# Kernel tuning notes

Hardware: AMD Instinct MI355X
Metric: run time of the kernel (lower is better)

## Reference

```python
import jax, jax.numpy as jnp
import numpy as np

B, S, INPUT_DIM = 8, 2048, 512
D_MODEL, N_LAYERS, OUTPUT_DIM = 1024, 6, 512
LAMBDA_INIT = 0.5


def _sinusoidal_pe(seq_len, d_model):
    # standard sinusoidal positional encoding, added over the sequence dim
    pos = np.arange(seq_len, dtype=np.float32)[:, None]
    div = np.exp(-np.log(10000.0) * np.arange(0, d_model, 2, dtype=np.float32) / d_model)
    pe = np.zeros((seq_len, d_model), dtype=np.float32)
    pe[:, 0::2] = np.sin(pos * div)
    pe[:, 1::2] = np.cos(pos * div)
    return jnp.asarray(pe)


def setup_inputs() -> dict:
    key = jax.random.key(0)
    ks = jax.random.split(key, 10)
    scale = 0.02
    x = jax.random.normal(ks[0], (B, S, INPUT_DIM), dtype=jnp.float32)
    W_in = jax.random.normal(ks[1], (D_MODEL, INPUT_DIM), dtype=jnp.float32) * scale
    b_in = jnp.zeros((D_MODEL,), dtype=jnp.float32)
    W_ctx = jax.random.normal(ks[2], (D_MODEL, D_MODEL), dtype=jnp.float32) * scale
    b_ctx = jnp.zeros((D_MODEL,), dtype=jnp.float32)
    # per-layer in_proj splits: W_q, W_k, W_v each [d_model, d_model]
    Wq = jax.random.normal(ks[3], (N_LAYERS, D_MODEL, D_MODEL), dtype=jnp.float32) * scale
    Wk = jax.random.normal(ks[4], (N_LAYERS, D_MODEL, D_MODEL), dtype=jnp.float32) * scale
    Wv = jax.random.normal(ks[5], (N_LAYERS, D_MODEL, D_MODEL), dtype=jnp.float32) * scale
    W_out = jax.random.normal(ks[6], (OUTPUT_DIM, D_MODEL), dtype=jnp.float32) * scale
    b_out = jnp.zeros((OUTPUT_DIM,), dtype=jnp.float32)
    return {"x": x, "W_in": W_in, "b_in": b_in, "W_ctx": W_ctx, "b_ctx": b_ctx,
            "Wq": Wq, "Wk": Wk, "Wv": Wv, "W_out": W_out, "b_out": b_out}


def _diff_attention(h, W_q, W_k, W_v):
    # h: [B, S, d]; weights used un-transposed, matching X @ W_q in the source
    d = h.shape[-1]
    half = d // 2
    Q = h @ W_q
    K = h @ W_k
    V = h @ W_v
    Q1, Q2 = Q[..., :half], Q[..., half:]
    K1, K2 = K[..., :half], K[..., half:]
    s = 1.0 / jnp.sqrt(jnp.float32(d))
    A1 = jnp.einsum('bqd,bkd->bqk', Q1, K1) * s  # [B, S, S]
    A2 = jnp.einsum('bqd,bkd->bqk', Q2, K2) * s
    scores = jax.nn.softmax(A1, axis=-1) - LAMBDA_INIT * jax.nn.softmax(A2, axis=-1)
    return jnp.einsum('bqk,bkd->bqd', scores, V)


def reference(x, W_in, b_in, W_ctx, b_ctx, Wq, Wk, Wv, W_out, b_out):
    h = x @ W_in.T + b_in            # input_fc
    h = h @ W_ctx.T + b_ctx          # context_embedding
    h = h + _sinusoidal_pe(S, D_MODEL)[None, :, :]
    for i in range(N_LAYERS):
        h = _diff_attention(h, Wq[i], Wk[i], Wv[i])
    return h @ W_out.T + b_out
```

## Files before the change

kernel.cpp:

```cpp
#include <hip/hip_runtime.h>
#include <stdint.h>

typedef unsigned short u16b;
typedef __attribute__((ext_vector_type(8))) __bf16 bf16x8;
typedef __attribute__((ext_vector_type(8))) unsigned short ushort8;
typedef __attribute__((ext_vector_type(4))) float f32x4;

#define B_    8
#define S_    2048
#define DIN_  512
#define DM_   1024
#define NL_   6
#define DOUT_ 512
#define MTOT  (B_ * S_)

__device__ __forceinline__ u16b f2bf(float f) {
  unsigned u = __builtin_bit_cast(unsigned, f);
  u += 0x7fffu + ((u >> 16) & 1u);
  return (u16b)(u >> 16);
}
__device__ __forceinline__ float bf2f(u16b h) {
  return __builtin_bit_cast(float, (unsigned)h << 16);
}

__global__ void pe_kernel(float* __restrict__ pe) {
  int idx = blockIdx.x * 256 + threadIdx.x;
  int s = idx >> 10, d = idx & 1023;
  int j = d >> 1;
  double div = exp(-log(10000.0) * (double)(2 * j) / 1024.0);
  double ang = (double)s * div;
  pe[idx] = (float)((d & 1) ? cos(ang) : sin(ang));
}

__global__ void cvt_bf16(const float* __restrict__ in, u16b* __restrict__ out, long long n) {
  long long i = (long long)blockIdx.x * 256 + threadIdx.x;
  long long st = (long long)gridDim.x * 256;
  for (; i < n; i += st) out[i] = f2bf(in[i]);
}

__global__ void tr3_f32_bf16(const float* __restrict__ q, const float* __restrict__ k,
                             const float* __restrict__ v,
                             u16b* __restrict__ oq, u16b* __restrict__ ok2,
                             u16b* __restrict__ ov) {
  __shared__ float tile[32][33];
  const float* in = blockIdx.z == 0 ? q : (blockIdx.z == 1 ? k : v);
  u16b* out = blockIdx.z == 0 ? oq : (blockIdx.z == 1 ? ok2 : ov);
  int c0 = blockIdx.x * 32, r0 = blockIdx.y * 32;
  int tx = threadIdx.x, ty = threadIdx.y;
#pragma unroll
  for (int i = 0; i < 4; ++i)
    tile[ty + i * 8][tx] = in[(size_t)(r0 + ty + i * 8) * DM_ + c0 + tx];
  __syncthreads();
#pragma unroll
  for (int i = 0; i < 4; ++i)
    out[(size_t)(c0 + ty + i * 8) * DM_ + r0 + tx] = f2bf(tile[tx][ty + i * 8]);
}

__global__ __launch_bounds__(256) void softmax_combine(const float* __restrict__ A1,
                                                       const float* __restrict__ A2,
                                                       u16b* __restrict__ P,
                                                       long long pstride) {
  size_t row = blockIdx.x;
  const float* a1 = A1 + row * 2048;
  const float* a2 = A2 + row * 2048;
  u16b* p = P + row * pstride;
  int t = threadIdx.x, w = t >> 6, lane = t & 63;
  float v1[8], v2[8];
  float m1 = -3.4e38f, m2 = -3.4e38f;
#pragma unroll
  for (int i = 0; i < 8; ++i) {
    v1[i] = a1[i * 256 + t];
    v2[i] = a2[i * 256 + t];
    m1 = fmaxf(m1, v1[i]);
    m2 = fmaxf(m2, v2[i]);
  }
  __shared__ float red1[4], red2[4];
#pragma unroll
  for (int o = 32; o; o >>= 1) {
    m1 = fmaxf(m1, __shfl_xor(m1, o));
    m2 = fmaxf(m2, __shfl_xor(m2, o));
  }
  if (lane == 0) { red1[w] = m1; red2[w] = m2; }
  __syncthreads();
  m1 = fmaxf(fmaxf(red1[0], red1[1]), fmaxf(red1[2], red1[3]));
  m2 = fmaxf(fmaxf(red2[0], red2[1]), fmaxf(red2[2], red2[3]));
  float s1 = 0.f, s2 = 0.f;
#pragma unroll
  for (int i = 0; i < 8; ++i) {
    v1[i] = expf(v1[i] - m1);
    v2[i] = expf(v2[i] - m2);
    s1 += v1[i];
    s2 += v2[i];
  }
#pragma unroll
  for (int o = 32; o; o >>= 1) {
    s1 += __shfl_xor(s1, o);
    s2 += __shfl_xor(s2, o);
  }
  __syncthreads();
  if (lane == 0) { red1[w] = s1; red2[w] = s2; }
  __syncthreads();
  s1 = red1[0] + red1[1] + red1[2] + red1[3];
  s2 = red2[0] + red2[1] + red2[2] + red2[3];
  float i1 = 1.0f / s1, i2 = 0.5f / s2;
#pragma unroll
  for (int i = 0; i < 8; ++i)
    p[i * 256 + t] = f2bf(v1[i] * i1 - v2[i] * i2);
}

__global__ __launch_bounds__(256) void softmax_quad(const u16b* __restrict__ A1b,
                                                    const u16b* __restrict__ A2b,
                                                    u16b* __restrict__ P, int quadBase) {
  int row = blockIdx.x;
  int bb = row >> 11, r = row & 2047;
  size_t ro = (size_t)bb * S_ * S_ + (size_t)r * S_;
  const u16b* a1 = A1b + ro;
  const u16b* a2 = A2b + ro;
  u16b* p = P + (size_t)(quadBase + bb) * S_ * S_ + (size_t)r * S_;
  int t = threadIdx.x, w = t >> 6, lane = t & 63;
  ushort8 x1 = *(const ushort8*)&a1[t * 8];
  ushort8 x2 = *(const ushort8*)&a2[t * 8];
  float v1[8], v2[8];
  float m1 = -3.4e38f, m2 = -3.4e38f;
#pragma unroll
  for (int i = 0; i < 8; ++i) {
    v1[i] = bf2f(x1[i]);
    v2[i] = bf2f(x2[i]);
    m1 = fmaxf(m1, v1[i]);
    m2 = fmaxf(m2, v2[i]);
  }
  __shared__ float red1[4], red2[4];
#pragma unroll
  for (int o = 32; o; o >>= 1) {
    m1 = fmaxf(m1, __shfl_xor(m1, o));
    m2 = fmaxf(m2, __shfl_xor(m2, o));
  }
  if (lane == 0) { red1[w] = m1; red2[w] = m2; }
  __syncthreads();
  m1 = fmaxf(fmaxf(red1[0], red1[1]), fmaxf(red1[2], red1[3]));
  m2 = fmaxf(fmaxf(red2[0], red2[1]), fmaxf(red2[2], red2[3]));
  float s1 = 0.f, s2 = 0.f;
#pragma unroll
  for (int i = 0; i < 8; ++i) {
    v1[i] = expf(v1[i] - m1);
    v2[i] = expf(v2[i] - m2);
    s1 += v1[i];
    s2 += v2[i];
  }
#pragma unroll
  for (int o = 32; o; o >>= 1) {
    s1 += __shfl_xor(s1, o);
    s2 += __shfl_xor(s2, o);
  }
  __syncthreads();
  if (lane == 0) { red1[w] = s1; red2[w] = s2; }
  __syncthreads();
  s1 = red1[0] + red1[1] + red1[2] + red1[3];
  s2 = red2[0] + red2[1] + red2[2] + red2[3];
  float i1 = 1.0f / s1, i2 = 0.5f / s2;
  ushort8 outv;
#pragma unroll
  for (int i = 0; i < 8; ++i) outv[i] = f2bf(v1[i] * i1 - v2[i] * i2);
  *(ushort8*)&p[t * 8] = outv;
}

#define GEPI_BF16      0
#define GEPI_BIAS      1
#define GEPI_BIAS_PE   2
#define GEPI_F32SCALE  3
#define GEPI_F32BIAS   4
#define GEPI_BF16_VT   5
#define GEPI_BF16SCALE 6

template <int EPI>
__global__ __launch_bounds__(256) void gemm_nt(
    const u16b* __restrict__ A, long long sAr, long long sAb,
    const u16b* __restrict__ Bt, long long sBr, long long sBb,
    void* __restrict__ Cv, long long sCr, long long sCb,
    int K, const float* __restrict__ bias, const float* __restrict__ pe, float alpha) {
  __shared__ __align__(16) u16b smem[16384];
  u16b* As = smem;
  u16b* Bs = smem + 8192;
  const int z = blockIdx.z;
  const u16b* Ab = A + (size_t)z * sAb;
  const u16b* Bb = Bt + (size_t)z * sBb;
  const int m0 = blockIdx.x * 128, n0 = blockIdx.y * 128;
  const int t = threadIdx.x;
  const int w = t >> 6, lane = t & 63;
  const int wr = w >> 1, wc = w & 1;
  const int lr = lane & 15, g0 = lane >> 4;

  f32x4 acc[4][4] = {};

  const int nkt = K >> 6;
  for (int kt = 0; kt < nkt; ++kt) {
#pragma unroll
    for (int i = 0; i < 4; ++i) {
      int c = i * 256 + t;
      int r = c >> 3, cc = c & 7;
      int gc = cc ^ (r & 7);
      const u16b* ga = Ab + (size_t)(m0 + r) * sAr + kt * 64 + gc * 8;
      const u16b* gb = Bb + (size_t)(n0 + r) * sBr + kt * 64 + gc * 8;
      u16b* la = &As[(i * 256 + w * 64) * 8];
      u16b* lb = &Bs[(i * 256 + w * 64) * 8];
      __builtin_amdgcn_global_load_lds((__attribute__((address_space(1))) void*)ga,
                                       (__attribute__((address_space(3))) void*)la, 16, 0, 0);
      __builtin_amdgcn_global_load_lds((__attribute__((address_space(1))) void*)gb,
                                       (__attribute__((address_space(3))) void*)lb, 16, 0, 0);
    }
    __syncthreads();
#pragma unroll
    for (int kk = 0; kk < 2; ++kk) {
      bf16x8 af[4], bfr[4];
#pragma unroll
      for (int m = 0; m < 4; ++m) {
        int r = wr * 64 + m * 16 + lr;
        int sidx = (kk * 4 + g0) ^ (r & 7);
        af[m] = *(const bf16x8*)&As[(r * 8 + sidx) * 8];
      }
#pragma unroll
      for (int n = 0; n < 4; ++n) {
        int r = wc * 64 + n * 16 + lr;
        int sidx = (kk * 4 + g0) ^ (r & 7);
        bfr[n] = *(const bf16x8*)&Bs[(r * 8 + sidx) * 8];
      }
#pragma unroll
      for (int m = 0; m < 4; ++m)
#pragma unroll
        for (int n = 0; n < 4; ++n)
          acc[m][n] = __builtin_amdgcn_mfma_f32_16x16x32_bf16(af[m], bfr[n], acc[m][n], 0, 0, 0);
    }
    __syncthreads();
  }

  u16b* Ch = (u16b*)Cv;
  float* Cf = (float*)Cv;
  const size_t cb = (size_t)z * sCb;
#pragma unroll
  for (int m = 0; m < 4; ++m) {
#pragma unroll
    for (int j = 0; j < 4; ++j) {
      int r = m0 + wr * 64 + m * 16 + g0 * 4 + j;
      size_t ro = cb + (size_t)r * sCr;
#pragma unroll
      for (int n = 0; n < 4; ++n) {
        int c = n0 + wc * 64 + n * 16 + lr;
        float v = acc[m][n][j];
        if constexpr (EPI == GEPI_BF16) Ch[ro + c] = f2bf(v);
        else if constexpr (EPI == GEPI_BIAS) Ch[ro + c] = f2bf(v + bias[c]);
        else if constexpr (EPI == GEPI_BIAS_PE)
          Ch[ro + c] = f2bf(v + bias[c] + pe[(size_t)(r & (S_ - 1)) * DM_ + c]);
        else if constexpr (EPI == GEPI_F32SCALE) Cf[ro + c] = v * alpha;
        else Cf[ro + c] = v + bias[c];
      }
    }
  }
}

template <int EPI>
__global__ __launch_bounds__(512, 1) void gemm8(
    const u16b* __restrict__ A, long long sAr, long long sAb, long long sAb2,
    const u16b* __restrict__ Bt, long long sBr, long long sBb, long long sBb2,
    void* __restrict__ Cv, long long sCr, long long sCb, long long sCb2,
    int K, const float* __restrict__ bias, const float* __restrict__ pe, float alpha) {
  extern __shared__ __align__(16) u16b lds[];
  const int z = blockIdx.z;
  const u16b* Ab = A + (size_t)(z >> 1) * sAb2 + (size_t)(z & 1) * sAb;
  const u16b* Bb = Bt + (size_t)(z >> 1) * sBb2 + (size_t)(z & 1) * sBb;
  const int m0 = blockIdx.x * 256, n0 = blockIdx.y * 256;
  const int t = threadIdx.x;
  const int wid = t >> 6, lane = t & 63;
  const int wr = wid >> 2, wc = wid & 3;
  const int lr = lane & 15, g0 = lane >> 4;

  f32x4 acc[8][4] = {};
  const int nkt = K >> 6;

  auto stage = [&](int kt, int buf) {
    u16b* bufA = lds + buf * 32768;
    u16b* bufB = bufA + 16384;
#pragma unroll
    for (int i = 0; i < 4; ++i) {
      int id = i * 512 + t;
      int r = id >> 3, cc = id & 7;
      int gc = cc ^ (r & 7);
      const u16b* ga = Ab + (size_t)(m0 + r) * sAr + kt * 64 + gc * 8;
      const u16b* gb = Bb + (size_t)(n0 + r) * sBr + kt * 64 + gc * 8;
      u16b* la = bufA + (i * 512 + wid * 64) * 8;
      u16b* lb = bufB + (i * 512 + wid * 64) * 8;
      __builtin_amdgcn_global_load_lds((__attribute__((address_space(1))) void*)ga,
                                       (__attribute__((address_space(3))) void*)la, 16, 0, 0);
      __builtin_amdgcn_global_load_lds((__attribute__((address_space(1))) void*)gb,
                                       (__attribute__((address_space(3))) void*)lb, 16, 0, 0);
    }
  };

  stage(0, 0);
  __builtin_amdgcn_sched_barrier(0);
  asm volatile("s_waitcnt vmcnt(0)" ::: "memory");
  __builtin_amdgcn_sched_barrier(0);
  __builtin_amdgcn_s_barrier();
  __builtin_amdgcn_sched_barrier(0);

  for (int kt = 0; kt < nkt; ++kt) {
    const int cur = kt & 1;
    if (kt + 1 < nkt) stage(kt + 1, cur ^ 1);
    __builtin_amdgcn_sched_barrier(0);
    const u16b* bufA = lds + cur * 32768;
    const u16b* bufB = bufA + 16384;
#pragma unroll
    for (int kk = 0; kk < 2; ++kk) {
      bf16x8 af[8], bfr[4];
#pragma unroll
      for (int m = 0; m < 8; ++m) {
        int r = wr * 128 + m * 16 + lr;
        int sidx = (kk * 4 + g0) ^ (r & 7);
        af[m] = *(const bf16x8*)&bufA[(r * 8 + sidx) * 8];
      }
#pragma unroll
      for (int n = 0; n < 4; ++n) {
        int r = wc * 64 + n * 16 + lr;
        int sidx = (kk * 4 + g0) ^ (r & 7);
        bfr[n] = *(const bf16x8*)&bufB[(r * 8 + sidx) * 8];
      }
      __builtin_amdgcn_s_setprio(1);
#pragma unroll
      for (int m = 0; m < 8; ++m)
#pragma unroll
        for (int n = 0; n < 4; ++n)
          acc[m][n] = __builtin_amdgcn_mfma_f32_16x16x32_bf16(af[m], bfr[n], acc[m][n], 0, 0, 0);
      __builtin_amdgcn_s_setprio(0);
    }
    __builtin_amdgcn_sched_barrier(0);
    asm volatile("s_waitcnt vmcnt(0)" ::: "memory");
    __builtin_amdgcn_sched_barrier(0);
    __builtin_amdgcn_s_barrier();
    __builtin_amdgcn_sched_barrier(0);
  }

  if constexpr (EPI == GEPI_BF16_VT) {
    u16b* tile = lds;
#pragma unroll
    for (int m = 0; m < 8; ++m)
#pragma unroll
      for (int j = 0; j < 4; ++j) {
        int rl = wr * 128 + m * 16 + g0 * 4 + j;
#pragma unroll
        for (int n = 0; n < 4; ++n) {
          int cl = wc * 64 + n * 16 + lr;
          tile[cl * 256 + (rl ^ ((cl & 7) << 3))] = f2bf(acc[m][n][j]);
        }
      }
    __syncthreads();
    u16b* vtb = (u16b*)Cv;
    const int batch = m0 >> 11;
    const int r0b = m0 & (S_ - 1);
    u16b* obase = vtb + (size_t)batch * DM_ * S_ + r0b;
#pragma unroll
    for (int it = 0; it < 16; ++it) {
      int id = it * 512 + t;
      int c = id >> 5, rc = id & 31;
      *(bf16x8*)&obase[(size_t)(n0 + c) * S_ + rc * 8] =
          *(const bf16x8*)&tile[c * 256 + ((rc * 8) ^ ((c & 7) << 3))];
    }
    return;
  }

  u16b* Ch = (u16b*)Cv;
  float* Cf = (float*)Cv;
  const size_t cb = (size_t)(z >> 1) * sCb2 + (size_t)(z & 1) * sCb;
#pragma unroll
  for (int m = 0; m < 8; ++m) {
#pragma unroll
    for (int j = 0; j < 4; ++j) {
      int r = m0 + wr * 128 + m * 16 + g0 * 4 + j;
      size_t ro = cb + (size_t)r * sCr;
#pragma unroll
      for (int n = 0; n < 4; ++n) {
        int c = n0 + wc * 64 + n * 16 + lr;
        float v = acc[m][n][j];
        if constexpr (EPI == GEPI_BF16) Ch[ro + c] = f2bf(v);
        else if constexpr (EPI == GEPI_BIAS) Ch[ro + c] = f2bf(v + bias[c]);
        else if constexpr (EPI == GEPI_BIAS_PE)
          Ch[ro + c] = f2bf(v + bias[c] + pe[(size_t)(r & (S_ - 1)) * DM_ + c]);
        else if constexpr (EPI == GEPI_F32SCALE) Cf[ro + c] = v * alpha;
        else if constexpr (EPI == GEPI_BF16SCALE) Ch[ro + c] = f2bf(v * alpha);
        else Cf[ro + c] = v + bias[c];
      }
    }
  }
}

extern "C" void kernel_launch(void* const* d_in, const int* in_sizes, int n_in,
                              void* d_out, int out_size, void* d_ws, size_t ws_size,
                              hipStream_t stream) {
  const float* x     = (const float*)d_in[0];
  const float* W_in  = (const float*)d_in[1];
  const float* b_in  = (const float*)d_in[2];
  const float* W_ctx = (const float*)d_in[3];
  const float* b_ctx = (const float*)d_in[4];
  const float* Wq    = (const float*)d_in[5];
  const float* Wk    = (const float*)d_in[6];
  const float* Wv    = (const float*)d_in[7];
  const float* W_out = (const float*)d_in[8];
  const float* b_out = (const float*)d_in[9];
  float* out = (float*)d_out;

  const int LDS8 = 131072;
  hipFuncSetAttribute((const void*)gemm8<GEPI_BF16>,
                      hipFuncAttributeMaxDynamicSharedMemorySize, LDS8);
  hipFuncSetAttribute((const void*)gemm8<GEPI_BIAS>,
                      hipFuncAttributeMaxDynamicSharedMemorySize, LDS8);
  hipFuncSetAttribute((const void*)gemm8<GEPI_BIAS_PE>,
                      hipFuncAttributeMaxDynamicSharedMemorySize, LDS8);
  hipFuncSetAttribute((const void*)gemm8<GEPI_BF16_VT>,
                      hipFuncAttributeMaxDynamicSharedMemorySize, LDS8);
  hipFuncSetAttribute((const void*)gemm8<GEPI_BF16SCALE>,
                      hipFuncAttributeMaxDynamicSharedMemorySize, LDS8);

  const size_t SZ_A12 = (size_t)2 * S_ * S_ * 4;
  const size_t SZ_PF  = (size_t)B_ * S_ * S_ * 2;
  const size_t SZ_H   = (size_t)MTOT * DM_ * 2;
  const size_t SZ_WIN = (size_t)DM_ * DIN_ * 2;
  const size_t SZ_WX  = (size_t)DM_ * DM_ * 2;
  const size_t SZ_WO  = (size_t)DOUT_ * DM_ * 2;
  const size_t SZ_WL  = (size_t)3 * DM_ * DM_ * 2;
  const size_t SLACK  = 65536;
  const size_t needB = SZ_A12 + SZ_PF + 4 * SZ_H + SZ_WO + SZ_WL + SLACK;
  const size_t needC = SZ_A12 + 4 * SZ_H + SZ_WIN + SZ_WX + SZ_WO + SZ_WL + SLACK;
  bool fullP = ws_size >= needB;
  if (ws_size < needC) return;

  char* wsp = (char*)d_ws;
  size_t off = 0;
  auto alloc = [&](size_t bytes) -> void* {
    void* p = wsp + off;
    off += (bytes + 255) & ~(size_t)255;
    return p;
  };
  float* A12  = (float*)alloc(SZ_A12);
  u16b* Pfull = fullP ? (u16b*)alloc(SZ_PF) : nullptr;
  u16b* hbuf  = (u16b*)alloc(SZ_H);
  u16b* qbuf  = (u16b*)alloc(SZ_H);
  u16b* kbuf  = (u16b*)alloc(SZ_H);
  u16b* vtb   = (u16b*)alloc(SZ_H);
  u16b *winb, *wctxb;
  if (fullP) {
    winb  = (u16b*)Pfull;
    wctxb = (u16b*)((char*)Pfull + SZ_WIN);
  } else {
    winb  = (u16b*)alloc(SZ_WIN);
    wctxb = (u16b*)alloc(SZ_WX);
  }
  u16b* woutb = (u16b*)alloc(SZ_WO);
  u16b* wTl   = (u16b*)alloc(SZ_WL);

  u16b* xbf = (u16b*)A12;
  float* pe = (float*)((char*)A12 + (size_t)MTOT * DIN_ * 2);
  float* A1f = A12;
  float* A2f = A12 + (size_t)S_ * S_;
  u16b* A12u = (u16b*)A12;

  const size_t WSTEP = (size_t)DM_ * DM_;
  u16b* wqTl = wTl;
  u16b* wkTl = wTl + WSTEP;
  u16b* wvTl = wTl + 2 * WSTEP;

  dim3 blk(256), trb(32, 8);

  pe_kernel<<<dim3((S_ * DM_) / 256), blk, 0, stream>>>(pe);
  cvt_bf16<<<dim3(2048), blk, 0, stream>>>(x, xbf, (long long)MTOT * DIN_);
  cvt_bf16<<<dim3(512), blk, 0, stream>>>(W_in, winb, (long long)DM_ * DIN_);
  cvt_bf16<<<dim3(1024), blk, 0, stream>>>(W_ctx, wctxb, (long long)DM_ * DM_);
  cvt_bf16<<<dim3(512), blk, 0, stream>>>(W_out, woutb, (long long)DOUT_ * DM_);

  gemm8<GEPI_BIAS><<<dim3(MTOT / 256, DM_ / 256, 1), dim3(512), LDS8, stream>>>(
      xbf, DIN_, 0, 0, winb, DIN_, 0, 0, qbuf, DM_, 0, 0, DIN_, b_in, nullptr, 1.0f);
  gemm8<GEPI_BIAS_PE><<<dim3(MTOT / 256, DM_ / 256, 1), dim3(512), LDS8, stream>>>(
      qbuf, DM_, 0, 0, wctxb, DM_, 0, 0, hbuf, DM_, 0, 0, DM_, b_ctx, pe, 1.0f);

  for (int l = 0; l < NL_; ++l) {
    tr3_f32_bf16<<<dim3(32, 32, 3), trb, 0, stream>>>(
        Wq + (size_t)l * WSTEP, Wk + (size_t)l * WSTEP, Wv + (size_t)l * WSTEP,
        wqTl, wkTl, wvTl);
    gemm8<GEPI_BF16><<<dim3(MTOT / 256, DM_ / 256, 2), dim3(512), LDS8, stream>>>(
        hbuf, DM_, 0, 0, wqTl, DM_, (long long)WSTEP, 0,
        qbuf, DM_, (long long)(kbuf - qbuf), 0, DM_, nullptr, nullptr, 1.0f);
    gemm8<GEPI_BF16_VT><<<dim3(MTOT / 256, DM_ / 256, 1), dim3(512), LDS8, stream>>>(
        hbuf, DM_, 0, 0, wvTl, DM_, 0, 0, vtb, 0, 0, 0, DM_, nullptr, nullptr, 1.0f);

    if (fullP) {
      for (int qd = 0; qd < 2; ++qd) {
        const u16b* qb = qbuf + (size_t)(4 * qd) * S_ * DM_;
        const u16b* kb = kbuf + (size_t)(4 * qd) * S_ * DM_;
        gemm8<GEPI_BF16SCALE><<<dim3(S_ / 256, S_ / 256, 8), dim3(512), LDS8, stream>>>(
            qb, DM_, DM_ / 2, (long long)S_ * DM_,
            kb, DM_, DM_ / 2, (long long)S_ * DM_,
            A12u, S_, (long long)(hbuf - A12u), (long long)S_ * S_,
            DM_ / 2, nullptr, nullptr, 0.03125f);
        softmax_quad<<<dim3(4 * S_), blk, 0, stream>>>(A12u, hbuf, Pfull, 4 * qd);
      }
      gemm8<GEPI_BF16><<<dim3(S_ / 256, DM_ / 256, B_), dim3(512), LDS8, stream>>>(
          Pfull, S_, (long long)S_ * S_, 2 * (long long)S_ * S_,
          vtb, S_, (long long)DM_ * S_, 2 * (long long)DM_ * S_,
          hbuf, DM_, (long long)S_ * DM_, 2 * (long long)S_ * DM_,
          S_, nullptr, nullptr, 1.0f);
    } else {
      for (int b = 0; b < B_; ++b) {
        const u16b* qb = qbuf + (size_t)b * S_ * DM_;
        const u16b* kb = kbuf + (size_t)b * S_ * DM_;
        gemm_nt<GEPI_F32SCALE><<<dim3(S_ / 128, S_ / 128, 2), blk, 0, stream>>>(
            qb, DM_, DM_ / 2, kb, DM_, DM_ / 2,
            A1f, S_, (long long)S_ * S_, DM_ / 2, nullptr, nullptr, 0.03125f);
        softmax_combine<<<dim3(S_), blk, 0, stream>>>(A1f, A2f, (u16b*)A1f, 2 * S_);
        gemm_nt<GEPI_BF16><<<dim3(S_ / 128, DM_ / 128, 1), blk, 0, stream>>>(
            (u16b*)A1f, 2 * S_, 0, vtb + (size_t)b * DM_ * S_, S_, 0,
            hbuf + (size_t)b * S_ * DM_, DM_, 0, S_, nullptr, nullptr, 1.0f);
      }
    }
  }

  gemm_nt<GEPI_F32BIAS><<<dim3(MTOT / 128, DOUT_ / 128, 1), blk, 0, stream>>>(
      hbuf, DM_, 0, woutb, DM_, 0, out, DOUT_, 0, DM_, b_out, nullptr, 1.0f);
}
```

Before: 1.814 ms.

## Interleave gemm8 prefetch with MFMA phases and merge score launches

The gemm8 main loop is split into four phases. Each phase loads part of the A fragments, issues a slice of the next k-tile's global-to-LDS loads, and runs its MFMAs, with partial vmcnt waits and barriers in between. The goal is to overlap global loads with compute more finely than a single full-tile prefetch. The attention score path also moves from two quad launches to one 16-batch GEMM plus a single in-place softmax, with buffers reordered so A1 lives in Pfull and A2 in the A12 region. This cuts launch count and a copy, but adds more barriers per k-tile and relies on the remapped buffers not overlapping.

```diff
diff --git a/kernel.cpp b/kernel.cpp
--- a/kernel.cpp
+++ b/kernel.cpp
@@ -108,15 +108,11 @@
     p[i * 256 + t] = f2bf(v1[i] * i1 - v2[i] * i2);
 }
 
-__global__ __launch_bounds__(256) void softmax_quad(const u16b* __restrict__ A1b,
-                                                    const u16b* __restrict__ A2b,
-                                                    u16b* __restrict__ P, int quadBase) {
-  int row = blockIdx.x;
-  int bb = row >> 11, r = row & 2047;
-  size_t ro = (size_t)bb * S_ * S_ + (size_t)r * S_;
-  const u16b* a1 = A1b + ro;
+__global__ __launch_bounds__(256) void softmax_full(u16b* __restrict__ A1b,
+                                                    const u16b* __restrict__ A2b) {
+  size_t ro = (size_t)blockIdx.x * S_;
+  u16b* a1 = A1b + ro;
   const u16b* a2 = A2b + ro;
-  u16b* p = P + (size_t)(quadBase + bb) * S_ * S_ + (size_t)r * S_;
   int t = threadIdx.x, w = t >> 6, lane = t & 63;
   ushort8 x1 = *(const ushort8*)&a1[t * 8];
   ushort8 x2 = *(const ushort8*)&a2[t * 8];
@@ -161,7 +157,7 @@
   ushort8 outv;
 #pragma unroll
   for (int i = 0; i < 8; ++i) outv[i] = f2bf(v1[i] * i1 - v2[i] * i2);
-  *(ushort8*)&p[t * 8] = outv;
+  *(ushort8*)&a1[t * 8] = outv;
 }
 
 #define GEPI_BF16      0
@@ -276,66 +272,84 @@
   f32x4 acc[8][4] = {};
   const int nkt = K >> 6;
 
-  auto stage = [&](int kt, int buf) {
-    u16b* bufA = lds + buf * 32768;
-    u16b* bufB = bufA + 16384;
-#pragma unroll
-    for (int i = 0; i < 4; ++i) {
-      int id = i * 512 + t;
-      int r = id >> 3, cc = id & 7;
-      int gc = cc ^ (r & 7);
-      const u16b* ga = Ab + (size_t)(m0 + r) * sAr + kt * 64 + gc * 8;
-      const u16b* gb = Bb + (size_t)(n0 + r) * sBr + kt * 64 + gc * 8;
-      u16b* la = bufA + (i * 512 + wid * 64) * 8;
-      u16b* lb = bufB + (i * 512 + wid * 64) * 8;
-      __builtin_amdgcn_global_load_lds((__attribute__((address_space(1))) void*)ga,
-                                       (__attribute__((address_space(3))) void*)la, 16, 0, 0);
-      __builtin_amdgcn_global_load_lds((__attribute__((address_space(1))) void*)gb,
-                                       (__attribute__((address_space(3))) void*)lb, 16, 0, 0);
-    }
+  auto stageUnit = [&](int kt, int buf, int isB, int i) {
+    int id = i * 512 + t;
+    int r = id >> 3, cc = id & 7;
+    int gc = cc ^ (r & 7);
+    const u16b* g = isB ? (Bb + (size_t)(n0 + r) * sBr + kt * 64 + gc * 8)
+                        : (Ab + (size_t)(m0 + r) * sAr + kt * 64 + gc * 8);
+    u16b* l = lds + buf * 32768 + (isB ? 16384 : 0) + (i * 512 + wid * 64) * 8;
+    __builtin_amdgcn_global_load_lds((__attribute__((address_space(1))) void*)g,
+                                     (__attribute__((address_space(3))) void*)l, 16, 0, 0);
   };
 
-  stage(0, 0);
-  __builtin_amdgcn_sched_barrier(0);
+#pragma unroll
+  for (int i = 0; i < 4; ++i) stageUnit(0, 0, 1, i);
+#pragma unroll
+  for (int i = 0; i < 4; ++i) stageUnit(0, 0, 0, i);
   asm volatile("s_waitcnt vmcnt(0)" ::: "memory");
   __builtin_amdgcn_sched_barrier(0);
   __builtin_amdgcn_s_barrier();
-  __builtin_amdgcn_sched_barrier(0);
 
   for (int kt = 0; kt < nkt; ++kt) {
     const int cur = kt & 1;
-    if (kt + 1 < nkt) stage(kt + 1, cur ^ 1);
-    __builtin_amdgcn_sched_barrier(0);
     const u16b* bufA = lds + cur * 32768;
     const u16b* bufB = bufA + 16384;
-#pragma unroll
-    for (int kk = 0; kk < 2; ++kk) {
-      bf16x8 af[8], bfr[4];
-#pragma unroll
-      for (int m = 0; m < 8; ++m) {
-        int r = wr * 128 + m * 16 + lr;
-        int sidx = (kk * 4 + g0) ^ (r & 7);
-        af[m] = *(const bf16x8*)&bufA[(r * 8 + sidx) * 8];
-      }
-#pragma unroll
-      for (int n = 0; n < 4; ++n) {
-        int r = wc * 64 + n * 16 + lr;
-        int sidx = (kk * 4 + g0) ^ (r & 7);
-        bfr[n] = *(const bf16x8*)&bufB[(r * 8 + sidx) * 8];
-      }
+    const bool pf = (kt + 1 < nkt);
+    bf16x8 bfr[4][2];
+#pragma unroll
+    for (int p = 0; p < 4; ++p) {
+      if (p == 0) {
+#pragma unroll
+        for (int n = 0; n < 4; ++n)
+#pragma unroll
+          for (int kk = 0; kk < 2; ++kk) {
+            int r = wc * 64 + n * 16 + lr;
+            int sidx = (kk * 4 + g0) ^ (r & 7);
+            bfr[n][kk] = *(const bf16x8*)&bufB[(r * 8 + sidx) * 8];
+          }
+      }
+      bf16x8 ap[2][2];
+#pragma unroll
+      for (int mm = 0; mm < 2; ++mm)
+#pragma unroll
+        for (int kk = 0; kk < 2; ++kk) {
+          int r = wr * 128 + (p * 2 + mm) * 16 + lr;
+          int sidx = (kk * 4 + g0) ^ (r & 7);
+          ap[mm][kk] = *(const bf16x8*)&bufA[(r * 8 + sidx) * 8];
+        }
+      if (pf) {
+        if (p == 0)      { stageUnit(kt + 1, cur ^ 1, 1, 0); stageUnit(kt + 1, cur ^ 1, 1, 2); }
+        else if (p == 1) { stageUnit(kt + 1, cur ^ 1, 1, 1); stageUnit(kt + 1, cur ^ 1, 1, 3); }
+        else if (p == 2) { stageUnit(kt + 1, cur ^ 1, 0, 0); stageUnit(kt + 1, cur ^ 1, 0, 2); }
+        else             { stageUnit(kt + 1, cur ^ 1, 0, 1); stageUnit(kt + 1, cur ^ 1, 0, 3); }
+      }
+      __builtin_amdgcn_sched_barrier(0);
+      __builtin_amdgcn_s_barrier();
+      asm volatile("s_waitcnt lgkmcnt(0)" ::: "memory");
+      __builtin_amdgcn_sched_barrier(0);
       __builtin_amdgcn_s_setprio(1);
 #pragma unroll
-      for (int m = 0; m < 8; ++m)
-#pragma unroll
-        for (int n = 0; n < 4; ++n)
-          acc[m][n] = __builtin_amdgcn_mfma_f32_16x16x32_bf16(af[m], bfr[n], acc[m][n], 0, 0, 0);
+      for (int kk = 0; kk < 2; ++kk)
+#pragma unroll
+        for (int mm = 0; mm < 2; ++mm)
+#pragma unroll
+          for (int n = 0; n < 4; ++n)
+            acc[p * 2 + mm][n] = __builtin_amdgcn_mfma_f32_16x16x32_bf16(
+                ap[mm][kk], bfr[n][kk], acc[p * 2 + mm][n], 0, 0, 0);
       __builtin_amdgcn_s_setprio(0);
-    }
-    __builtin_amdgcn_sched_barrier(0);
-    asm volatile("s_waitcnt vmcnt(0)" ::: "memory");
-    __builtin_amdgcn_sched_barrier(0);
-    __builtin_amdgcn_s_barrier();
-    __builtin_amdgcn_sched_barrier(0);
+      __builtin_amdgcn_sched_barrier(0);
+      if (p == 1) {
+        if (pf) asm volatile("s_waitcnt vmcnt(4)" ::: "memory");
+        else    asm volatile("s_waitcnt vmcnt(0)" ::: "memory");
+        __builtin_amdgcn_sched_barrier(0);
+      } else if (p == 3) {
+        if (pf) asm volatile("s_waitcnt vmcnt(2)" ::: "memory");
+        else    asm volatile("s_waitcnt vmcnt(0)" ::: "memory");
+        __builtin_amdgcn_sched_barrier(0);
+      }
+      __builtin_amdgcn_s_barrier();
+    }
   }
 
   if constexpr (EPI == GEPI_BF16_VT) {
@@ -438,8 +452,8 @@
     off += (bytes + 255) & ~(size_t)255;
     return p;
   };
+  u16b* Pfull = fullP ? (u16b*)alloc(SZ_PF) : nullptr;
   float* A12  = (float*)alloc(SZ_A12);
-  u16b* Pfull = fullP ? (u16b*)alloc(SZ_PF) : nullptr;
   u16b* hbuf  = (u16b*)alloc(SZ_H);
   u16b* qbuf  = (u16b*)alloc(SZ_H);
   u16b* kbuf  = (u16b*)alloc(SZ_H);
@@ -459,7 +473,7 @@
   float* pe = (float*)((char*)A12 + (size_t)MTOT * DIN_ * 2);
   float* A1f = A12;
   float* A2f = A12 + (size_t)S_ * S_;
-  u16b* A12u = (u16b*)A12;
+  u16b* A2u  = (u16b*)A12;
 
   const size_t WSTEP = (size_t)DM_ * DM_;
   u16b* wqTl = wTl;
@@ -490,16 +504,12 @@
         hbuf, DM_, 0, 0, wvTl, DM_, 0, 0, vtb, 0, 0, 0, DM_, nullptr, nullptr, 1.0f);
 
     if (fullP) {
-      for (int qd = 0; qd < 2; ++qd) {
-        const u16b* qb = qbuf + (size_t)(4 * qd) * S_ * DM_;
-        const u16b* kb = kbuf + (size_t)(4 * qd) * S_ * DM_;
-        gemm8<GEPI_BF16SCALE><<<dim3(S_ / 256, S_ / 256, 8), dim3(512), LDS8, stream>>>(
-            qb, DM_, DM_ / 2, (long long)S_ * DM_,
-            kb, DM_, DM_ / 2, (long long)S_ * DM_,
-            A12u, S_, (long long)(hbuf - A12u), (long long)S_ * S_,
-            DM_ / 2, nullptr, nullptr, 0.03125f);
-        softmax_quad<<<dim3(4 * S_), blk, 0, stream>>>(A12u, hbuf, Pfull, 4 * qd);
-      }
+      gemm8<GEPI_BF16SCALE><<<dim3(S_ / 256, S_ / 256, 16), dim3(512), LDS8, stream>>>(
+          qbuf, DM_, DM_ / 2, (long long)S_ * DM_,
+          kbuf, DM_, DM_ / 2, (long long)S_ * DM_,
+          Pfull, S_, (long long)(A2u - Pfull), (long long)S_ * S_,
+          DM_ / 2, nullptr, nullptr, 0.03125f);
+      softmax_full<<<dim3(MTOT), blk, 0, stream>>>(Pfull, A2u);
       gemm8<GEPI_BF16><<<dim3(S_ / 256, DM_ / 256, B_), dim3(512), LDS8, stream>>>(
           Pfull, S_, (long long)S_ * S_, 2 * (long long)S_ * S_,
           vtb, S_, (long long)DM_ * S_, 2 * (long long)DM_ * S_,
```

Result: slower. 1.895 ms (+4.5%).

## Fuse QKV projections into one launch and batch all score GEMMs with in-place softmax

Applied to the files above, without the earlier changes.

The Q/K and V projection GEMMs are merged into a single launch with z=3, where the z==2 slice writes transposed V through a repurposed pointer argument. The per-quad loop of score GEMM plus softmax is replaced by one 16-slice score GEMM over all batches. A1 is written directly into the P buffer and A2 into scratch, and softmax then overwrites A1 in place. This cuts launch count and tail effects, and drops the separate P write target, at the cost of larger scratch buffers being live together and some pointer aliasing tricks.

```diff
diff --git a/kernel.cpp b/kernel.cpp
--- a/kernel.cpp
+++ b/kernel.cpp
@@ -108,15 +108,11 @@
     p[i * 256 + t] = f2bf(v1[i] * i1 - v2[i] * i2);
 }
 
-__global__ __launch_bounds__(256) void softmax_quad(const u16b* __restrict__ A1b,
-                                                    const u16b* __restrict__ A2b,
-                                                    u16b* __restrict__ P, int quadBase) {
-  int row = blockIdx.x;
-  int bb = row >> 11, r = row & 2047;
-  size_t ro = (size_t)bb * S_ * S_ + (size_t)r * S_;
-  const u16b* a1 = A1b + ro;
+__global__ __launch_bounds__(256) void softmax_full(u16b* __restrict__ A1b,
+                                                    const u16b* __restrict__ A2b) {
+  size_t ro = (size_t)blockIdx.x * S_;
+  u16b* a1 = A1b + ro;
   const u16b* a2 = A2b + ro;
-  u16b* p = P + (size_t)(quadBase + bb) * S_ * S_ + (size_t)r * S_;
   int t = threadIdx.x, w = t >> 6, lane = t & 63;
   ushort8 x1 = *(const ushort8*)&a1[t * 8];
   ushort8 x2 = *(const ushort8*)&a2[t * 8];
@@ -161,7 +157,7 @@
   ushort8 outv;
 #pragma unroll
   for (int i = 0; i < 8; ++i) outv[i] = f2bf(v1[i] * i1 - v2[i] * i2);
-  *(ushort8*)&p[t * 8] = outv;
+  *(ushort8*)&a1[t * 8] = outv;
 }
 
 #define GEPI_BF16      0
@@ -171,6 +167,7 @@
 #define GEPI_F32BIAS   4
 #define GEPI_BF16_VT   5
 #define GEPI_BF16SCALE 6
+#define GEPI_QKV       7
 
 template <int EPI>
 __global__ __launch_bounds__(256) void gemm_nt(
@@ -338,8 +335,10 @@
     __builtin_amdgcn_sched_barrier(0);
   }
 
-  if constexpr (EPI == GEPI_BF16_VT) {
+  const bool doVT = (EPI == GEPI_BF16_VT) || (EPI == GEPI_QKV && z == 2);
+  if (doVT) {
     u16b* tile = lds;
+    u16b* vtb = (EPI == GEPI_QKV) ? (u16b*)(void*)pe : (u16b*)Cv;
 #pragma unroll
     for (int m = 0; m < 8; ++m)
 #pragma unroll
@@ -352,7 +351,6 @@
         }
       }
     __syncthreads();
-    u16b* vtb = (u16b*)Cv;
     const int batch = m0 >> 11;
     const int r0b = m0 & (S_ - 1);
     u16b* obase = vtb + (size_t)batch * DM_ * S_ + r0b;
@@ -379,7 +377,7 @@
       for (int n = 0; n < 4; ++n) {
         int c = n0 + wc * 64 + n * 16 + lr;
         float v = acc[m][n][j];
-        if constexpr (EPI == GEPI_BF16) Ch[ro + c] = f2bf(v);
+        if constexpr (EPI == GEPI_BF16 || EPI == GEPI_QKV) Ch[ro + c] = f2bf(v);
         else if constexpr (EPI == GEPI_BIAS) Ch[ro + c] = f2bf(v + bias[c]);
         else if constexpr (EPI == GEPI_BIAS_PE)
           Ch[ro + c] = f2bf(v + bias[c] + pe[(size_t)(r & (S_ - 1)) * DM_ + c]);
@@ -413,7 +411,7 @@
                       hipFuncAttributeMaxDynamicSharedMemorySize, LDS8);
   hipFuncSetAttribute((const void*)gemm8<GEPI_BIAS_PE>,
                       hipFuncAttributeMaxDynamicSharedMemorySize, LDS8);
-  hipFuncSetAttribute((const void*)gemm8<GEPI_BF16_VT>,
+  hipFuncSetAttribute((const void*)gemm8<GEPI_QKV>,
                       hipFuncAttributeMaxDynamicSharedMemorySize, LDS8);
   hipFuncSetAttribute((const void*)gemm8<GEPI_BF16SCALE>,
                       hipFuncAttributeMaxDynamicSharedMemorySize, LDS8);
@@ -438,8 +436,8 @@
     off += (bytes + 255) & ~(size_t)255;
     return p;
   };
+  u16b* Pfull = fullP ? (u16b*)alloc(SZ_PF) : nullptr;
   float* A12  = (float*)alloc(SZ_A12);
-  u16b* Pfull = fullP ? (u16b*)alloc(SZ_PF) : nullptr;
   u16b* hbuf  = (u16b*)alloc(SZ_H);
   u16b* qbuf  = (u16b*)alloc(SZ_H);
   u16b* kbuf  = (u16b*)alloc(SZ_H);
@@ -459,7 +457,7 @@
   float* pe = (float*)((char*)A12 + (size_t)MTOT * DIN_ * 2);
   float* A1f = A12;
   float* A2f = A12 + (size_t)S_ * S_;
-  u16b* A12u = (u16b*)A12;
+  u16b* A2u  = (u16b*)A12;
 
   const size_t WSTEP = (size_t)DM_ * DM_;
   u16b* wqTl = wTl;
@@ -483,23 +481,17 @@
     tr3_f32_bf16<<<dim3(32, 32, 3), trb, 0, stream>>>(
         Wq + (size_t)l * WSTEP, Wk + (size_t)l * WSTEP, Wv + (size_t)l * WSTEP,
         wqTl, wkTl, wvTl);
-    gemm8<GEPI_BF16><<<dim3(MTOT / 256, DM_ / 256, 2), dim3(512), LDS8, stream>>>(
-        hbuf, DM_, 0, 0, wqTl, DM_, (long long)WSTEP, 0,
-        qbuf, DM_, (long long)(kbuf - qbuf), 0, DM_, nullptr, nullptr, 1.0f);
-    gemm8<GEPI_BF16_VT><<<dim3(MTOT / 256, DM_ / 256, 1), dim3(512), LDS8, stream>>>(
-        hbuf, DM_, 0, 0, wvTl, DM_, 0, 0, vtb, 0, 0, 0, DM_, nullptr, nullptr, 1.0f);
+    gemm8<GEPI_QKV><<<dim3(MTOT / 256, DM_ / 256, 3), dim3(512), LDS8, stream>>>(
+        hbuf, DM_, 0, 0, wqTl, DM_, (long long)WSTEP, 2 * (long long)WSTEP,
+        qbuf, DM_, (long long)(kbuf - qbuf), 0, DM_, nullptr, (const float*)vtb, 1.0f);
 
     if (fullP) {
-      for (int qd = 0; qd < 2; ++qd) {
-        const u16b* qb = qbuf + (size_t)(4 * qd) * S_ * DM_;
-        const u16b* kb = kbuf + (size_t)(4 * qd) * S_ * DM_;
-        gemm8<GEPI_BF16SCALE><<<dim3(S_ / 256, S_ / 256, 8), dim3(512), LDS8, stream>>>(
-            qb, DM_, DM_ / 2, (long long)S_ * DM_,
-            kb, DM_, DM_ / 2, (long long)S_ * DM_,
-            A12u, S_, (long long)(hbuf - A12u), (long long)S_ * S_,
-            DM_ / 2, nullptr, nullptr, 0.03125f);
-        softmax_quad<<<dim3(4 * S_), blk, 0, stream>>>(A12u, hbuf, Pfull, 4 * qd);
-      }
+      gemm8<GEPI_BF16SCALE><<<dim3(S_ / 256, S_ / 256, 16), dim3(512), LDS8, stream>>>(
+          qbuf, DM_, DM_ / 2, (long long)S_ * DM_,
+          kbuf, DM_, DM_ / 2, (long long)S_ * DM_,
+          Pfull, S_, (long long)(A2u - Pfull), (long long)S_ * S_,
+          DM_ / 2, nullptr, nullptr, 0.03125f);
+      softmax_full<<<dim3(MTOT), blk, 0, stream>>>(Pfull, A2u);
       gemm8<GEPI_BF16><<<dim3(S_ / 256, DM_ / 256, B_), dim3(512), LDS8, stream>>>(
           Pfull, S_, (long long)S_ * S_, 2 * (long long)S_ * S_,
           vtb, S_, (long long)DM_ * S_, 2 * (long long)DM_ * S_,
```

Measured after the change: 1.770 ms. 2.4% less time.
